# Kernel optimization log

Hardware: AMD Instinct MI355X
Metric: run time of the kernel (lower is better)

Reference implementation:

```python
import jax, jax.numpy as jnp
import numpy as np

B, T, C, H = 2, 2048, 1024, 16
D = C // H  # head dim


def setup_inputs() -> dict:
    key = jax.random.key(0)
    ks = jax.random.split(key, 8)
    s = 1.0 / np.sqrt(C)
    return {
        "x_q": jax.random.normal(ks[0], (B, T, C), jnp.float32),
        "x_kv": jax.random.normal(ks[1], (B, T, C), jnp.float32),
        "Wq": jax.random.normal(ks[2], (C, C), jnp.float32) * s,
        "bq": jnp.zeros((C,), jnp.float32),
        "Wkv": jax.random.normal(ks[3], (C, 2 * C), jnp.float32) * s,
        "bkv": jnp.zeros((2 * C,), jnp.float32),
        "Wo": jax.random.normal(ks[4], (C, C), jnp.float32) * s,
        "bo": jnp.zeros((C,), jnp.float32),
    }


def reference(x_q, x_kv, Wq, bq, Wkv, bkv, Wo, bo):
    q = x_q @ Wq + bq                      # [B,Tq,C]
    kv = x_kv @ Wkv + bkv                  # [B,Tkv,2C]
    k, v = kv[..., :C], kv[..., C:]
    # split heads -> [B,H,T,D]
    q = q.reshape(B, T, H, D).transpose(0, 2, 1, 3)
    k = k.reshape(B, T, H, D).transpose(0, 2, 1, 3)
    v = v.reshape(B, T, H, D).transpose(0, 2, 1, 3)
    att = jnp.einsum("bhqd,bhkd->bhqk", q, k) * (1.0 / np.sqrt(D))
    att = jax.nn.softmax(att, axis=-1)
    y = jnp.einsum("bhqk,bhkd->bhqd", att, v)
    y = y.transpose(0, 2, 1, 3).reshape(B, T, C)
    return y @ Wo + bo
```

## Files before the change

### kernel.cpp

```cpp
#include <hip/hip_runtime.h>

#define NB 2
#define NT 2048
#define NC 1024
#define NH 16
#define ND 64
#define NC2 2048
#define QSCALE (0.125f * 1.4426950408889634f)

typedef __attribute__((ext_vector_type(8))) __bf16 bf16x8;
typedef __attribute__((ext_vector_type(8))) unsigned short ushort8;
typedef __attribute__((ext_vector_type(4))) float f32x4;

__device__ __forceinline__ unsigned short bf16_bits(float f) {
  union { float f; unsigned int u; } x; x.f = f;
  unsigned int r = x.u + 0x7fffu + ((x.u >> 16) & 1u);
  return (unsigned short)(r >> 16);
}
__device__ __forceinline__ float bf2f(unsigned short u) {
  union { unsigned int u; float f; } x; x.u = ((unsigned int)u) << 16;
  return x.f;
}
__device__ __forceinline__ void g2l16(const void* g, void* l) {
  __builtin_amdgcn_global_load_lds(
      (const __attribute__((address_space(1))) unsigned int*)g,
      (__attribute__((address_space(3))) unsigned int*)l, 16, 0, 0);
}
__device__ __forceinline__ bf16x8 ld8(const unsigned short* p) {
  return *(const bf16x8*)p;
}
__device__ __forceinline__ unsigned int cvtpk(float lo, float hi) {
  unsigned int r;
  asm("v_cvt_pk_bf16_f32 %0, %1, %2" : "=v"(r) : "v"(lo), "v"(hi));
  return r;
}
__device__ __forceinline__ float vexp2(float x) {
  float r;
  asm("v_exp_f32 %0, %1" : "=v"(r) : "v"(x));
  return r;
}

__device__ __forceinline__ int wave_is_f32(const unsigned short* __restrict__ x) {
  const int lane = threadIdx.x & 63;
  ulonglong2 v = ((const ulonglong2*)x)[lane];
  const unsigned short* u = (const unsigned short*)&v;
  int c = 0;
#pragma unroll
  for (int k = 0; k < 8; ++k) {
    int e = (u[k] >> 7) & 0xFF;
    c += (e != 0 && (e < 112 || e > 142)) ? 1 : 0;
  }
#pragma unroll
  for (int off = 32; off > 0; off >>= 1) c += __shfl_down(c, off);
  return __shfl(c, 0) > 64;
}

__global__ __launch_bounds__(256) void prep(const void* __restrict__ xq,
                                            const void* __restrict__ xkv,
                                            const void* __restrict__ w0,
                                            const void* __restrict__ w1,
                                            const void* __restrict__ w2,
                                            unsigned short* __restrict__ oq,
                                            unsigned short* __restrict__ okv,
                                            unsigned short* __restrict__ o0,
                                            unsigned short* __restrict__ o1,
                                            unsigned short* __restrict__ o2) {
  __shared__ unsigned short tile[32][33];
  const int bx = blockIdx.x, by = blockIdx.y;
  const int f = wave_is_f32((const unsigned short*)xq);
  if (bx < 128) {
    if (!f) return;
    const int fb = bx * 32 + by;
    const void* in = (fb < 2048) ? xq : xkv;
    unsigned short* out = (fb < 2048) ? oq : okv;
    const int i = (fb & 2047) * 256 + threadIdx.x;
    const float4* p = (const float4*)in;
    float4 a = p[i * 2], b = p[i * 2 + 1];
    ushort8 o;
    o[0] = bf16_bits(a.x); o[1] = bf16_bits(a.y); o[2] = bf16_bits(a.z); o[3] = bf16_bits(a.w);
    o[4] = bf16_bits(b.x); o[5] = bf16_bits(b.y); o[6] = bf16_bits(b.z); o[7] = bf16_bits(b.w);
    *(ushort8*)&out[(size_t)i * 8] = o;
  } else {
    const int tb = bx - 128;
    const void* in; unsigned short* out; int cols, cb;
    if (tb < 32)      { in = w0; out = o0; cols = NC;  cb = tb; }
    else if (tb < 96) { in = w1; out = o1; cols = NC2; cb = tb - 32; }
    else              { in = w2; out = o2; cols = NC;  cb = tb - 96; }
    const int c0 = cb * 32, r0 = by * 32;
    const int tx = threadIdx.x & 31, ty = threadIdx.x >> 5;
#pragma unroll
    for (int i = 0; i < 32; i += 8) {
      size_t idx = (size_t)(r0 + ty + i) * cols + c0 + tx;
      tile[ty + i][tx] = f ? bf16_bits(((const float*)in)[idx]) : ((const unsigned short*)in)[idx];
    }
    __syncthreads();
#pragma unroll
    for (int i = 0; i < 32; i += 8)
      out[(size_t)(c0 + ty + i) * NC + r0 + tx] = tile[tx][ty + i];
  }
}

__global__ __launch_bounds__(256) void gemm_qkv(const unsigned short* __restrict__ xq_raw,
                                                const unsigned short* __restrict__ xkv_raw,
                                                const unsigned short* __restrict__ xq_cvt,
                                                const unsigned short* __restrict__ xkv_cvt,
                                                const unsigned short* __restrict__ Wqt,
                                                const unsigned short* __restrict__ Wkvt,
                                                const void* __restrict__ bq,
                                                const void* __restrict__ bkv,
                                                unsigned short* __restrict__ qb,
                                                unsigned short* __restrict__ kf2,
                                                unsigned short* __restrict__ vt2) {
  __shared__ unsigned short As[128][64];
  __shared__ unsigned short Bs[128][64];
  const int f = wave_is_f32(xq_raw);
  const bool isq = blockIdx.y < 8;
  const unsigned short* A  = isq ? (f ? xq_cvt : xq_raw) : (f ? xkv_cvt : xkv_raw);
  const unsigned short* Bt = isq ? Wqt : Wkvt;
  const int m0 = blockIdx.x * 128;
  const int n0 = (isq ? blockIdx.y : blockIdx.y - 8) * 128;
  const int tid = threadIdx.x, w = tid >> 6, lane = tid & 63;
  const int lrow = lane & 15, lhi = lane >> 4;
  const int wr = w >> 1, wc = w & 1;
  const int grow = lane >> 3, gcol = (lane & 7) * 8;
  f32x4 acc[4][4] = {};
  for (int k0 = 0; k0 < NC; k0 += 64) {
    __syncthreads();
#pragma unroll
    for (int p = 0; p < 4; ++p) {
      const int r = w * 32 + p * 8;
      g2l16(&A[(size_t)(m0 + r + grow) * NC + k0 + gcol], &As[r][0]);
      g2l16(&Bt[(size_t)(n0 + r + grow) * NC + k0 + gcol], &Bs[r][0]);
    }
    __syncthreads();
    bf16x8 af[2][4], bfr[2][4];
#pragma unroll
    for (int kk = 0; kk < 2; ++kk) {
#pragma unroll
      for (int i = 0; i < 4; ++i)
        af[kk][i] = ld8(&As[wr * 64 + i * 16 + lrow][kk * 32 + lhi * 8]);
#pragma unroll
      for (int j = 0; j < 4; ++j)
        bfr[kk][j] = ld8(&Bs[wc * 64 + j * 16 + lrow][kk * 32 + lhi * 8]);
    }
#pragma unroll
    for (int kk = 0; kk < 2; ++kk)
#pragma unroll
      for (int i = 0; i < 4; ++i)
#pragma unroll
        for (int j = 0; j < 4; ++j)
          acc[i][j] = __builtin_amdgcn_mfma_f32_16x16x32_bf16(af[kk][i], bfr[kk][j], acc[i][j], 0, 0, 0);
  }
  const void* bias = isq ? bq : bkv;
  if (!isq && n0 >= NC) {
#pragma unroll
    for (int j = 0; j < 4; ++j) {
      const int col = n0 + wc * 64 + j * 16 + lrow;
      const float bj = f ? ((const float*)bias)[col] : bf2f(((const unsigned short*)bias)[col]);
#pragma unroll
      for (int i = 0; i < 4; ++i) {
        const int row = m0 + wr * 64 + i * 16 + lhi * 4;
        float v[4];
#pragma unroll
        for (int r = 0; r < 4; ++r) v[r] = acc[i][j][r] + bj;
        const int cv = col - NC;
        const int hV = cv >> 6, dcol = cv & 63;
        const int bV = row >> 11, tt = row & 2047;
        const size_t base = ((size_t)((bV * NH + hV) * 32 + (tt >> 6))) * 4096
                          + (dcol >> 4) * 1024 + ((tt >> 4) & 1) * 512
                          + (((tt >> 2) & 3) * 16 + (dcol & 15)) * 8 + ((tt >> 5) & 1) * 4;
        ushort4 o4;
        o4.x = bf16_bits(v[0]); o4.y = bf16_bits(v[1]);
        o4.z = bf16_bits(v[2]); o4.w = bf16_bits(v[3]);
        *(ushort4*)&vt2[base] = o4;
      }
    }
  } else {
    __syncthreads();
    unsigned short* Cw = &As[0][0] + w * 1280;
    const int rowbase = m0 + wr * 64;
    const int hK = (n0 + wc * 64) >> 6;
    const size_t tb = ((size_t)(((rowbase >> 11) * NH + hK) * 32 + ((rowbase & 2047) >> 6))) * 4096;
#pragma unroll
    for (int i = 0; i < 4; ++i) {
#pragma unroll
      for (int j = 0; j < 4; ++j) {
        const int col = n0 + wc * 64 + j * 16 + lrow;
        const float bj = f ? ((const float*)bias)[col] : bf2f(((const unsigned short*)bias)[col]);
#pragma unroll
        for (int r = 0; r < 4; ++r) {
          const float v = acc[i][j][r] + bj;
          Cw[(lhi * 4 + r) * 72 + j * 16 + lrow] = bf16_bits(isq ? v * QSCALE : v);
        }
      }
      if (isq) {
#pragma unroll
        for (int p = 0; p < 2; ++p) {
          const int row_l = p * 8 + (lane >> 3), col_l = (lane & 7) * 8;
          const bf16x8 v8 = ld8(&Cw[row_l * 72 + col_l]);
          *(bf16x8*)&qb[(size_t)(rowbase + i * 16 + row_l) * NC + n0 + wc * 64 + col_l] = v8;
        }
      } else {
#pragma unroll
        for (int p = 0; p < 2; ++p) {
          const bf16x8 v8 = ld8(&Cw[(lane & 15) * 72 + p * 32 + (lane >> 4) * 8]);
          *(bf16x8*)&kf2[tb + i * 1024 + p * 512 + lane * 8] = v8;
        }
      }
    }
  }
}

__global__ __launch_bounds__(256) void gemm_out(const unsigned short* __restrict__ A,
                                                const unsigned short* __restrict__ Bt,
                                                const void* __restrict__ bias,
                                                void* __restrict__ Cout,
                                                const unsigned short* __restrict__ xdet) {
  __shared__ unsigned short As[128][64];
  __shared__ unsigned short Bs[128][64];
  const int f = wave_is_f32(xdet);
  const int m0 = blockIdx.x * 128, n0 = blockIdx.y * 128;
  const int tid = threadIdx.x, w = tid >> 6, lane = tid & 63;
  const int lrow = lane & 15, lhi = lane >> 4;
  const int wr = w >> 1, wc = w & 1;
  const int grow = lane >> 3, gcol = (lane & 7) * 8;
  f32x4 acc[4][4] = {};
  for (int k0 = 0; k0 < NC; k0 += 64) {
    __syncthreads();
#pragma unroll
    for (int p = 0; p < 4; ++p) {
      const int r = w * 32 + p * 8;
      g2l16(&A[(size_t)(m0 + r + grow) * NC + k0 + gcol], &As[r][0]);
      g2l16(&Bt[(size_t)(n0 + r + grow) * NC + k0 + gcol], &Bs[r][0]);
    }
    __syncthreads();
    bf16x8 af[2][4], bfr[2][4];
#pragma unroll
    for (int kk = 0; kk < 2; ++kk) {
#pragma unroll
      for (int i = 0; i < 4; ++i)
        af[kk][i] = ld8(&As[wr * 64 + i * 16 + lrow][kk * 32 + lhi * 8]);
#pragma unroll
      for (int j = 0; j < 4; ++j)
        bfr[kk][j] = ld8(&Bs[wc * 64 + j * 16 + lrow][kk * 32 + lhi * 8]);
    }
#pragma unroll
    for (int kk = 0; kk < 2; ++kk)
#pragma unroll
      for (int i = 0; i < 4; ++i)
#pragma unroll
        for (int j = 0; j < 4; ++j)
          acc[i][j] = __builtin_amdgcn_mfma_f32_16x16x32_bf16(af[kk][i], bfr[kk][j], acc[i][j], 0, 0, 0);
  }
#pragma unroll
  for (int j = 0; j < 4; ++j) {
    const int col = n0 + wc * 64 + j * 16 + lrow;
    const float bj = f ? ((const float*)bias)[col] : bf2f(((const unsigned short*)bias)[col]);
#pragma unroll
    for (int i = 0; i < 4; ++i) {
      const int row = m0 + wr * 64 + i * 16 + lhi * 4;
#pragma unroll
      for (int r = 0; r < 4; ++r) {
        const float v = acc[i][j][r] + bj;
        const size_t idx = (size_t)(row + r) * NC + col;
        if (f) ((float*)Cout)[idx] = v;
        else ((unsigned short*)Cout)[idx] = bf16_bits(v);
      }
    }
  }
}

__global__ __launch_bounds__(128) void flash_attn(const unsigned short* __restrict__ q,
                                                  const unsigned short* __restrict__ kf2,
                                                  const unsigned short* __restrict__ vt2,
                                                  unsigned short* __restrict__ y) {
  const int fid = blockIdx.x + (blockIdx.y << 5);
  const int swz = ((fid & 7) << 7) + (fid >> 3);
  const int qt = swz & 31, bh = swz >> 5;
  const int b = bh >> 4, h = bh & 15;
  const int tid = threadIdx.x, w = tid >> 6, lane = tid & 63;
  const int lq = lane & 15, lhi = lane >> 4;

  bf16x8 qfA[2], qfB[2];
  {
    const unsigned short* qpA = q + (size_t)(b * NT + qt * 64 + w * 32 + lq) * NC + h * ND + lhi * 8;
    qfA[0] = ld8(qpA); qfA[1] = ld8(qpA + 32);
    qfB[0] = ld8(qpA + (size_t)16 * NC); qfB[1] = ld8(qpA + (size_t)16 * NC + 32);
  }
  f32x4 accA[4] = {}, accB[4] = {};
  float lA = 0.f, lB = 0.f;
  const unsigned short* kbase = kf2 + ((size_t)bh * 32) * 4096 + (size_t)lane * 8;
  const unsigned short* vbase = vt2 + ((size_t)bh * 32) * 4096 + (size_t)lane * 8;

#define KLOAD(kt_)                                                              \
  {                                                                             \
    _Pragma("unroll") for (int j = 0; j < 4; ++j)                               \
      _Pragma("unroll") for (int kk = 0; kk < 2; ++kk)                          \
        kR[j][kk] = ld8(kbase + (size_t)(kt_)*4096 + j * 1024 + kk * 512);      \
  }
#define VLOAD(kt_, V_)                                                          \
  {                                                                             \
    _Pragma("unroll") for (int jd = 0; jd < 4; ++jd)                            \
      _Pragma("unroll") for (int jj = 0; jj < 2; ++jj)                          \
        V_[jd][jj] = ld8(vbase + (size_t)(kt_)*4096 + jd * 1024 + jj * 512);    \
  }
#define TILE_BODY(it_, VC_, VN_)                                                  \
  {                                                                               \
    f32x4 sA[4], sB[4];                                                           \
    _Pragma("unroll") for (int j = 0; j < 4; ++j) {                               \
      f32x4 a = {}, bb2 = {};                                                     \
      _Pragma("unroll") for (int kk = 0; kk < 2; ++kk) {                          \
        a   = __builtin_amdgcn_mfma_f32_16x16x32_bf16(kR[j][kk], qfA[kk], a, 0, 0, 0);   \
        bb2 = __builtin_amdgcn_mfma_f32_16x16x32_bf16(kR[j][kk], qfB[kk], bb2, 0, 0, 0); \
      }                                                                           \
      sA[j] = a; sB[j] = bb2;                                                     \
    }                                                                             \
    if ((it_) + 1 < 32) KLOAD((it_) + 1);                                         \
    if ((it_) + 1 < 32) VLOAD((it_) + 1, VN_);                                    \
    float rsA = 0.f, rsB = 0.f;                                                   \
    _Pragma("unroll") for (int j = 0; j < 4; ++j)                                 \
      _Pragma("unroll") for (int r = 0; r < 4; ++r) {                             \
        const float pa = vexp2(sA[j][r]); sA[j][r] = pa; rsA += pa;               \
        const float pb = vexp2(sB[j][r]); sB[j][r] = pb; rsB += pb;               \
      }                                                                           \
    rsA += __shfl_xor(rsA, 16); rsA += __shfl_xor(rsA, 32);                       \
    rsB += __shfl_xor(rsB, 16); rsB += __shfl_xor(rsB, 32);                       \
    lA += rsA; lB += rsB;                                                         \
    union U { unsigned int u[4]; bf16x8 v; };                                     \
    U pA0, pA1, pB0, pB1;                                                         \
    pA0.u[0] = cvtpk(sA[0][0], sA[0][1]); pA0.u[1] = cvtpk(sA[0][2], sA[0][3]);   \
    pA0.u[2] = cvtpk(sA[2][0], sA[2][1]); pA0.u[3] = cvtpk(sA[2][2], sA[2][3]);   \
    pA1.u[0] = cvtpk(sA[1][0], sA[1][1]); pA1.u[1] = cvtpk(sA[1][2], sA[1][3]);   \
    pA1.u[2] = cvtpk(sA[3][0], sA[3][1]); pA1.u[3] = cvtpk(sA[3][2], sA[3][3]);   \
    pB0.u[0] = cvtpk(sB[0][0], sB[0][1]); pB0.u[1] = cvtpk(sB[0][2], sB[0][3]);   \
    pB0.u[2] = cvtpk(sB[2][0], sB[2][1]); pB0.u[3] = cvtpk(sB[2][2], sB[2][3]);   \
    pB1.u[0] = cvtpk(sB[1][0], sB[1][1]); pB1.u[1] = cvtpk(sB[1][2], sB[1][3]);   \
    pB1.u[2] = cvtpk(sB[3][0], sB[3][1]); pB1.u[3] = cvtpk(sB[3][2], sB[3][3]);   \
    __builtin_amdgcn_s_setprio(1);                                                \
    _Pragma("unroll") for (int jd = 0; jd < 4; ++jd) {                            \
      accA[jd] = __builtin_amdgcn_mfma_f32_16x16x32_bf16(VC_[jd][0], pA0.v, accA[jd], 0, 0, 0); \
      accA[jd] = __builtin_amdgcn_mfma_f32_16x16x32_bf16(VC_[jd][1], pA1.v, accA[jd], 0, 0, 0); \
      accB[jd] = __builtin_amdgcn_mfma_f32_16x16x32_bf16(VC_[jd][0], pB0.v, accB[jd], 0, 0, 0); \
      accB[jd] = __builtin_amdgcn_mfma_f32_16x16x32_bf16(VC_[jd][1], pB1.v, accB[jd], 0, 0, 0); \
    }                                                                             \
    __builtin_amdgcn_s_setprio(0);                                                \
  }

  bf16x8 kR[4][2];
  bf16x8 vRa[4][2], vRb[4][2];
  KLOAD(0);
  VLOAD(0, vRa);

  for (int itp = 0; itp < 16; ++itp) {
    const int it0 = itp * 2;
    TILE_BODY(it0, vRa, vRb);
    TILE_BODY(it0 + 1, vRb, vRa);
  }
#undef KLOAD
#undef VLOAD
#undef TILE_BODY

  const float invA = 1.f / lA, invB = 1.f / lB;
#pragma unroll
  for (int jd = 0; jd < 4; ++jd) {
    uint2 oA, oB;
    oA.x = cvtpk(accA[jd][0] * invA, accA[jd][1] * invA);
    oA.y = cvtpk(accA[jd][2] * invA, accA[jd][3] * invA);
    oB.x = cvtpk(accB[jd][0] * invB, accB[jd][1] * invB);
    oB.y = cvtpk(accB[jd][2] * invB, accB[jd][3] * invB);
    const size_t base = (size_t)(b * NT + qt * 64 + w * 32 + lq) * NC + h * ND + jd * 16 + lhi * 4;
    *(uint2*)&y[base] = oA;
    *(uint2*)&y[base + (size_t)16 * NC] = oB;
  }
}

extern "C" void kernel_launch(void* const* d_in, const int* in_sizes, int n_in,
                              void* d_out, int out_size, void* d_ws, size_t ws_size,
                              hipStream_t stream) {
  (void)in_sizes; (void)n_in; (void)out_size; (void)ws_size;
  char* ws = (char*)d_ws;
  unsigned short* xq_b  = (unsigned short*)(ws);
  unsigned short* xkv_b = (unsigned short*)(ws + ((size_t)8  << 20));
  unsigned short* Wqt   = (unsigned short*)(ws + ((size_t)16 << 20));
  unsigned short* Wkvt  = (unsigned short*)(ws + ((size_t)18 << 20));
  unsigned short* Wot   = (unsigned short*)(ws + ((size_t)22 << 20));
  unsigned short* qb    = (unsigned short*)(ws + ((size_t)24 << 20));
  unsigned short* kf2   = (unsigned short*)(ws + ((size_t)32 << 20));
  unsigned short* vt2   = (unsigned short*)(ws + ((size_t)48 << 20));
  unsigned short* yb    = (unsigned short*)(ws + ((size_t)56 << 20));
  const unsigned short* xdet = (const unsigned short*)d_in[0];

  prep<<<dim3(256, 32), 256, 0, stream>>>(d_in[0], d_in[1], d_in[2], d_in[4], d_in[6],
                                          xq_b, xkv_b, Wqt, Wkvt, Wot);
  gemm_qkv<<<dim3(32, 24), 256, 0, stream>>>((const unsigned short*)d_in[0],
                                             (const unsigned short*)d_in[1],
                                             xq_b, xkv_b, Wqt, Wkvt, d_in[3], d_in[5],
                                             qb, kf2, vt2);
  flash_attn<<<dim3(32, 32), 128, 0, stream>>>(qb, kf2, vt2, yb);
  gemm_out<<<dim3(32, 8), 256, 0, stream>>>(yb, Wot, d_in[7], d_out, xdet);
}
```

Measured before the change: 140.0 us.

## Swizzle GEMM LDS tiles and give each attention wave all 64 query rows

Both projection GEMMs now XOR-swizzle the 16-byte column chunks in shared memory, in the global-to-LDS copy and in the fragment reads, so that fragment reads no longer hit the same LDS banks. The flash attention kernel drops from two waves per block to one. That single wave processes four 16-row query groups against each loaded K/V tile, so each K/V register load is reused four times instead of twice. The trade-off is fewer waves in flight per block, higher register pressure from four accumulator sets, and removal of the V double buffering, which may expose load latency.

```diff
diff --git a/kernel.cpp b/kernel.cpp
--- a/kernel.cpp
+++ b/kernel.cpp
@@ -122,15 +122,17 @@
   const int tid = threadIdx.x, w = tid >> 6, lane = tid & 63;
   const int lrow = lane & 15, lhi = lane >> 4;
   const int wr = w >> 1, wc = w & 1;
-  const int grow = lane >> 3, gcol = (lane & 7) * 8;
+  const int grow = lane >> 3;
+  const int gc = (((lane & 7) ^ grow) * 8);
+  const int rg = (lrow & 7);
   f32x4 acc[4][4] = {};
   for (int k0 = 0; k0 < NC; k0 += 64) {
     __syncthreads();
 #pragma unroll
     for (int p = 0; p < 4; ++p) {
       const int r = w * 32 + p * 8;
-      g2l16(&A[(size_t)(m0 + r + grow) * NC + k0 + gcol], &As[r][0]);
-      g2l16(&Bt[(size_t)(n0 + r + grow) * NC + k0 + gcol], &Bs[r][0]);
+      g2l16(&A[(size_t)(m0 + r + grow) * NC + k0 + gc], &As[r][0]);
+      g2l16(&Bt[(size_t)(n0 + r + grow) * NC + k0 + gc], &Bs[r][0]);
     }
     __syncthreads();
     bf16x8 af[2][4], bfr[2][4];
@@ -138,10 +140,10 @@
     for (int kk = 0; kk < 2; ++kk) {
 #pragma unroll
       for (int i = 0; i < 4; ++i)
-        af[kk][i] = ld8(&As[wr * 64 + i * 16 + lrow][kk * 32 + lhi * 8]);
+        af[kk][i] = ld8(&As[wr * 64 + i * 16 + lrow][((kk * 4 + lhi) ^ rg) * 8]);
 #pragma unroll
       for (int j = 0; j < 4; ++j)
-        bfr[kk][j] = ld8(&Bs[wc * 64 + j * 16 + lrow][kk * 32 + lhi * 8]);
+        bfr[kk][j] = ld8(&Bs[wc * 64 + j * 16 + lrow][((kk * 4 + lhi) ^ rg) * 8]);
     }
 #pragma unroll
     for (int kk = 0; kk < 2; ++kk)
@@ -223,15 +225,17 @@
   const int tid = threadIdx.x, w = tid >> 6, lane = tid & 63;
   const int lrow = lane & 15, lhi = lane >> 4;
   const int wr = w >> 1, wc = w & 1;
-  const int grow = lane >> 3, gcol = (lane & 7) * 8;
+  const int grow = lane >> 3;
+  const int gc = (((lane & 7) ^ grow) * 8);
+  const int rg = (lrow & 7);
   f32x4 acc[4][4] = {};
   for (int k0 = 0; k0 < NC; k0 += 64) {
     __syncthreads();
 #pragma unroll
     for (int p = 0; p < 4; ++p) {
       const int r = w * 32 + p * 8;
-      g2l16(&A[(size_t)(m0 + r + grow) * NC + k0 + gcol], &As[r][0]);
-      g2l16(&Bt[(size_t)(n0 + r + grow) * NC + k0 + gcol], &Bs[r][0]);
+      g2l16(&A[(size_t)(m0 + r + grow) * NC + k0 + gc], &As[r][0]);
+      g2l16(&Bt[(size_t)(n0 + r + grow) * NC + k0 + gc], &Bs[r][0]);
     }
     __syncthreads();
     bf16x8 af[2][4], bfr[2][4];
@@ -239,10 +243,10 @@
     for (int kk = 0; kk < 2; ++kk) {
 #pragma unroll
       for (int i = 0; i < 4; ++i)
-        af[kk][i] = ld8(&As[wr * 64 + i * 16 + lrow][kk * 32 + lhi * 8]);
+        af[kk][i] = ld8(&As[wr * 64 + i * 16 + lrow][((kk * 4 + lhi) ^ rg) * 8]);
 #pragma unroll
       for (int j = 0; j < 4; ++j)
-        bfr[kk][j] = ld8(&Bs[wc * 64 + j * 16 + lrow][kk * 32 + lhi * 8]);
+        bfr[kk][j] = ld8(&Bs[wc * 64 + j * 16 + lrow][((kk * 4 + lhi) ^ rg) * 8]);
     }
 #pragma unroll
     for (int kk = 0; kk < 2; ++kk)
@@ -270,107 +274,141 @@
   }
 }
 
-__global__ __launch_bounds__(128) void flash_attn(const unsigned short* __restrict__ q,
-                                                  const unsigned short* __restrict__ kf2,
-                                                  const unsigned short* __restrict__ vt2,
-                                                  unsigned short* __restrict__ y) {
+__global__ __launch_bounds__(64) void flash_attn(const unsigned short* __restrict__ q,
+                                                 const unsigned short* __restrict__ kf2,
+                                                 const unsigned short* __restrict__ vt2,
+                                                 unsigned short* __restrict__ y) {
   const int fid = blockIdx.x + (blockIdx.y << 5);
   const int swz = ((fid & 7) << 7) + (fid >> 3);
   const int qt = swz & 31, bh = swz >> 5;
   const int b = bh >> 4, h = bh & 15;
-  const int tid = threadIdx.x, w = tid >> 6, lane = tid & 63;
+  const int lane = threadIdx.x;
   const int lq = lane & 15, lhi = lane >> 4;
 
-  bf16x8 qfA[2], qfB[2];
+  bf16x8 qf0[2], qf1[2], qf2[2], qf3[2];
   {
-    const unsigned short* qpA = q + (size_t)(b * NT + qt * 64 + w * 32 + lq) * NC + h * ND + lhi * 8;
-    qfA[0] = ld8(qpA); qfA[1] = ld8(qpA + 32);
-    qfB[0] = ld8(qpA + (size_t)16 * NC); qfB[1] = ld8(qpA + (size_t)16 * NC + 32);
-  }
-  f32x4 accA[4] = {}, accB[4] = {};
-  float lA = 0.f, lB = 0.f;
+    const unsigned short* qp = q + (size_t)(b * NT + qt * 64 + lq) * NC + h * ND + lhi * 8;
+    qf0[0] = ld8(qp);                      qf0[1] = ld8(qp + 32);
+    qf1[0] = ld8(qp + (size_t)16 * NC);    qf1[1] = ld8(qp + (size_t)16 * NC + 32);
+    qf2[0] = ld8(qp + (size_t)32 * NC);    qf2[1] = ld8(qp + (size_t)32 * NC + 32);
+    qf3[0] = ld8(qp + (size_t)48 * NC);    qf3[1] = ld8(qp + (size_t)48 * NC + 32);
+  }
+  f32x4 acc0[4] = {}, acc1[4] = {}, acc2[4] = {}, acc3[4] = {};
+  float l0 = 0.f, l1 = 0.f, l2 = 0.f, l3 = 0.f;
   const unsigned short* kbase = kf2 + ((size_t)bh * 32) * 4096 + (size_t)lane * 8;
   const unsigned short* vbase = vt2 + ((size_t)bh * 32) * 4096 + (size_t)lane * 8;
 
+  bf16x8 kR[4][2], vR[4][2];
 #define KLOAD(kt_)                                                              \
   {                                                                             \
     _Pragma("unroll") for (int j = 0; j < 4; ++j)                               \
       _Pragma("unroll") for (int kk = 0; kk < 2; ++kk)                          \
         kR[j][kk] = ld8(kbase + (size_t)(kt_)*4096 + j * 1024 + kk * 512);      \
   }
-#define VLOAD(kt_, V_)                                                          \
+#define VLOAD(kt_)                                                              \
   {                                                                             \
     _Pragma("unroll") for (int jd = 0; jd < 4; ++jd)                            \
       _Pragma("unroll") for (int jj = 0; jj < 2; ++jj)                          \
-        V_[jd][jj] = ld8(vbase + (size_t)(kt_)*4096 + jd * 1024 + jj * 512);    \
-  }
-#define TILE_BODY(it_, VC_, VN_)                                                  \
+        vR[jd][jj] = ld8(vbase + (size_t)(kt_)*4096 + jd * 1024 + jj * 512);    \
+  }
+#define GROUP(QF_, ACC_, L_)                                                      \
   {                                                                               \
-    f32x4 sA[4], sB[4];                                                           \
-    _Pragma("unroll") for (int j = 0; j < 4; ++j) {                               \
-      f32x4 a = {}, bb2 = {};                                                     \
-      _Pragma("unroll") for (int kk = 0; kk < 2; ++kk) {                          \
-        a   = __builtin_amdgcn_mfma_f32_16x16x32_bf16(kR[j][kk], qfA[kk], a, 0, 0, 0);   \
-        bb2 = __builtin_amdgcn_mfma_f32_16x16x32_bf16(kR[j][kk], qfB[kk], bb2, 0, 0, 0); \
-      }                                                                           \
-      sA[j] = a; sB[j] = bb2;                                                     \
+    f32x4 s0 = {}, s1 = {}, s2 = {}, s3 = {};                                     \
+    s0 = __builtin_amdgcn_mfma_f32_16x16x32_bf16(kR[0][0], QF_[0], s0, 0, 0, 0);  \
+    s0 = __builtin_amdgcn_mfma_f32_16x16x32_bf16(kR[0][1], QF_[1], s0, 0, 0, 0);  \
+    s1 = __builtin_amdgcn_mfma_f32_16x16x32_bf16(kR[1][0], QF_[0], s1, 0, 0, 0);  \
+    s1 = __builtin_amdgcn_mfma_f32_16x16x32_bf16(kR[1][1], QF_[1], s1, 0, 0, 0);  \
+    s2 = __builtin_amdgcn_mfma_f32_16x16x32_bf16(kR[2][0], QF_[0], s2, 0, 0, 0);  \
+    s2 = __builtin_amdgcn_mfma_f32_16x16x32_bf16(kR[2][1], QF_[1], s2, 0, 0, 0);  \
+    s3 = __builtin_amdgcn_mfma_f32_16x16x32_bf16(kR[3][0], QF_[0], s3, 0, 0, 0);  \
+    s3 = __builtin_amdgcn_mfma_f32_16x16x32_bf16(kR[3][1], QF_[1], s3, 0, 0, 0);  \
+    float rs = 0.f;                                                               \
+    _Pragma("unroll") for (int r = 0; r < 4; ++r) {                               \
+      s0[r] = vexp2(s0[r]); rs += s0[r];                                          \
+      s1[r] = vexp2(s1[r]); rs += s1[r];                                          \
+      s2[r] = vexp2(s2[r]); rs += s2[r];                                          \
+      s3[r] = vexp2(s3[r]); rs += s3[r];                                          \
     }                                                                             \
-    if ((it_) + 1 < 32) KLOAD((it_) + 1);                                         \
-    if ((it_) + 1 < 32) VLOAD((it_) + 1, VN_);                                    \
-    float rsA = 0.f, rsB = 0.f;                                                   \
-    _Pragma("unroll") for (int j = 0; j < 4; ++j)                                 \
-      _Pragma("unroll") for (int r = 0; r < 4; ++r) {                             \
-        const float pa = vexp2(sA[j][r]); sA[j][r] = pa; rsA += pa;               \
-        const float pb = vexp2(sB[j][r]); sB[j][r] = pb; rsB += pb;               \
-      }                                                                           \
-    rsA += __shfl_xor(rsA, 16); rsA += __shfl_xor(rsA, 32);                       \
-    rsB += __shfl_xor(rsB, 16); rsB += __shfl_xor(rsB, 32);                       \
-    lA += rsA; lB += rsB;                                                         \
+    rs += __shfl_xor(rs, 16); rs += __shfl_xor(rs, 32);                           \
+    L_ += rs;                                                                     \
     union U { unsigned int u[4]; bf16x8 v; };                                     \
-    U pA0, pA1, pB0, pB1;                                                         \
-    pA0.u[0] = cvtpk(sA[0][0], sA[0][1]); pA0.u[1] = cvtpk(sA[0][2], sA[0][3]);   \
-    pA0.u[2] = cvtpk(sA[2][0], sA[2][1]); pA0.u[3] = cvtpk(sA[2][2], sA[2][3]);   \
-    pA1.u[0] = cvtpk(sA[1][0], sA[1][1]); pA1.u[1] = cvtpk(sA[1][2], sA[1][3]);   \
-    pA1.u[2] = cvtpk(sA[3][0], sA[3][1]); pA1.u[3] = cvtpk(sA[3][2], sA[3][3]);   \
-    pB0.u[0] = cvtpk(sB[0][0], sB[0][1]); pB0.u[1] = cvtpk(sB[0][2], sB[0][3]);   \
-    pB0.u[2] = cvtpk(sB[2][0], sB[2][1]); pB0.u[3] = cvtpk(sB[2][2], sB[2][3]);   \
-    pB1.u[0] = cvtpk(sB[1][0], sB[1][1]); pB1.u[1] = cvtpk(sB[1][2], sB[1][3]);   \
-    pB1.u[2] = cvtpk(sB[3][0], sB[3][1]); pB1.u[3] = cvtpk(sB[3][2], sB[3][3]);   \
+    U p0, p1;                                                                     \
+    p0.u[0] = cvtpk(s0[0], s0[1]); p0.u[1] = cvtpk(s0[2], s0[3]);                 \
+    p0.u[2] = cvtpk(s2[0], s2[1]); p0.u[3] = cvtpk(s2[2], s2[3]);                 \
+    p1.u[0] = cvtpk(s1[0], s1[1]); p1.u[1] = cvtpk(s1[2], s1[3]);                 \
+    p1.u[2] = cvtpk(s3[0], s3[1]); p1.u[3] = cvtpk(s3[2], s3[3]);                 \
     __builtin_amdgcn_s_setprio(1);                                                \
     _Pragma("unroll") for (int jd = 0; jd < 4; ++jd) {                            \
-      accA[jd] = __builtin_amdgcn_mfma_f32_16x16x32_bf16(VC_[jd][0], pA0.v, accA[jd], 0, 0, 0); \
-      accA[jd] = __builtin_amdgcn_mfma_f32_16x16x32_bf16(VC_[jd][1], pA1.v, accA[jd], 0, 0, 0); \
-      accB[jd] = __builtin_amdgcn_mfma_f32_16x16x32_bf16(VC_[jd][0], pB0.v, accB[jd], 0, 0, 0); \
-      accB[jd] = __builtin_amdgcn_mfma_f32_16x16x32_bf16(VC_[jd][1], pB1.v, accB[jd], 0, 0, 0); \
+      ACC_[jd] = __builtin_amdgcn_mfma_f32_16x16x32_bf16(vR[jd][0], p0.v, ACC_[jd], 0, 0, 0); \
+      ACC_[jd] = __builtin_amdgcn_mfma_f32_16x16x32_bf16(vR[jd][1], p1.v, ACC_[jd], 0, 0, 0); \
     }                                                                             \
     __builtin_amdgcn_s_setprio(0);                                                \
   }
 
-  bf16x8 kR[4][2];
-  bf16x8 vRa[4][2], vRb[4][2];
   KLOAD(0);
-  VLOAD(0, vRa);
-
-  for (int itp = 0; itp < 16; ++itp) {
-    const int it0 = itp * 2;
-    TILE_BODY(it0, vRa, vRb);
-    TILE_BODY(it0 + 1, vRb, vRa);
+  VLOAD(0);
+  for (int kt = 0; kt < 32; ++kt) {
+    GROUP(qf0, acc0, l0);
+    GROUP(qf1, acc1, l1);
+    GROUP(qf2, acc2, l2);
+    {
+      f32x4 s0 = {}, s1 = {}, s2 = {}, s3 = {};
+      s0 = __builtin_amdgcn_mfma_f32_16x16x32_bf16(kR[0][0], qf3[0], s0, 0, 0, 0);
+      s0 = __builtin_amdgcn_mfma_f32_16x16x32_bf16(kR[0][1], qf3[1], s0, 0, 0, 0);
+      s1 = __builtin_amdgcn_mfma_f32_16x16x32_bf16(kR[1][0], qf3[0], s1, 0, 0, 0);
+      s1 = __builtin_amdgcn_mfma_f32_16x16x32_bf16(kR[1][1], qf3[1], s1, 0, 0, 0);
+      s2 = __builtin_amdgcn_mfma_f32_16x16x32_bf16(kR[2][0], qf3[0], s2, 0, 0, 0);
+      s2 = __builtin_amdgcn_mfma_f32_16x16x32_bf16(kR[2][1], qf3[1], s2, 0, 0, 0);
+      s3 = __builtin_amdgcn_mfma_f32_16x16x32_bf16(kR[3][0], qf3[0], s3, 0, 0, 0);
+      s3 = __builtin_amdgcn_mfma_f32_16x16x32_bf16(kR[3][1], qf3[1], s3, 0, 0, 0);
+      if (kt + 1 < 32) KLOAD(kt + 1);
+      float rs = 0.f;
+#pragma unroll
+      for (int r = 0; r < 4; ++r) {
+        s0[r] = vexp2(s0[r]); rs += s0[r];
+        s1[r] = vexp2(s1[r]); rs += s1[r];
+        s2[r] = vexp2(s2[r]); rs += s2[r];
+        s3[r] = vexp2(s3[r]); rs += s3[r];
+      }
+      rs += __shfl_xor(rs, 16); rs += __shfl_xor(rs, 32);
+      l3 += rs;
+      union U { unsigned int u[4]; bf16x8 v; };
+      U p0, p1;
+      p0.u[0] = cvtpk(s0[0], s0[1]); p0.u[1] = cvtpk(s0[2], s0[3]);
+      p0.u[2] = cvtpk(s2[0], s2[1]); p0.u[3] = cvtpk(s2[2], s2[3]);
+      p1.u[0] = cvtpk(s1[0], s1[1]); p1.u[1] = cvtpk(s1[2], s1[3]);
+      p1.u[2] = cvtpk(s3[0], s3[1]); p1.u[3] = cvtpk(s3[2], s3[3]);
+      __builtin_amdgcn_s_setprio(1);
+#pragma unroll
+      for (int jd = 0; jd < 4; ++jd) {
+        acc3[jd] = __builtin_amdgcn_mfma_f32_16x16x32_bf16(vR[jd][0], p0.v, acc3[jd], 0, 0, 0);
+        acc3[jd] = __builtin_amdgcn_mfma_f32_16x16x32_bf16(vR[jd][1], p1.v, acc3[jd], 0, 0, 0);
+      }
+      __builtin_amdgcn_s_setprio(0);
+    }
+    if (kt + 1 < 32) VLOAD(kt + 1);
   }
 #undef KLOAD
 #undef VLOAD
-#undef TILE_BODY
-
-  const float invA = 1.f / lA, invB = 1.f / lB;
+#undef GROUP
+
+  const float i0 = 1.f / l0, i1 = 1.f / l1, i2 = 1.f / l2, i3 = 1.f / l3;
+  const size_t base0 = (size_t)(b * NT + qt * 64 + lq) * NC + h * ND + lhi * 4;
 #pragma unroll
   for (int jd = 0; jd < 4; ++jd) {
-    uint2 oA, oB;
-    oA.x = cvtpk(accA[jd][0] * invA, accA[jd][1] * invA);
-    oA.y = cvtpk(accA[jd][2] * invA, accA[jd][3] * invA);
-    oB.x = cvtpk(accB[jd][0] * invB, accB[jd][1] * invB);
-    oB.y = cvtpk(accB[jd][2] * invB, accB[jd][3] * invB);
-    const size_t base = (size_t)(b * NT + qt * 64 + w * 32 + lq) * NC + h * ND + jd * 16 + lhi * 4;
-    *(uint2*)&y[base] = oA;
-    *(uint2*)&y[base + (size_t)16 * NC] = oB;
+    uint2 o;
+    o.x = cvtpk(acc0[jd][0] * i0, acc0[jd][1] * i0);
+    o.y = cvtpk(acc0[jd][2] * i0, acc0[jd][3] * i0);
+    *(uint2*)&y[base0 + jd * 16] = o;
+    o.x = cvtpk(acc1[jd][0] * i1, acc1[jd][1] * i1);
+    o.y = cvtpk(acc1[jd][2] * i1, acc1[jd][3] * i1);
+    *(uint2*)&y[base0 + (size_t)16 * NC + jd * 16] = o;
+    o.x = cvtpk(acc2[jd][0] * i2, acc2[jd][1] * i2);
+    o.y = cvtpk(acc2[jd][2] * i2, acc2[jd][3] * i2);
+    *(uint2*)&y[base0 + (size_t)32 * NC + jd * 16] = o;
+    o.x = cvtpk(acc3[jd][0] * i3, acc3[jd][1] * i3);
+    o.y = cvtpk(acc3[jd][2] * i3, acc3[jd][3] * i3);
+    *(uint2*)&y[base0 + (size_t)48 * NC + jd * 16] = o;
   }
 }
 
@@ -396,6 +434,6 @@
                                              (const unsigned short*)d_in[1],
                                              xq_b, xkv_b, Wqt, Wkvt, d_in[3], d_in[5],
                                              qb, kf2, vt2);
-  flash_attn<<<dim3(32, 32), 128, 0, stream>>>(qb, kf2, vt2, yb);
+  flash_attn<<<dim3(32, 32), 64, 0, stream>>>(qb, kf2, vt2, yb);
   gemm_out<<<dim3(32, 8), 256, 0, stream>>>(yb, Wot, d_in[7], d_out, xdet);
 }
```

Result: faster. 136.7 us (-2.4%).
